# Optimization experiments

Hardware: AMD Instinct MI355X
Metric: run time of the kernel (lower is better)

Reference implementation:

```python
import jax, jax.numpy as jnp
import numpy as np

B, D, L, G, K, U, OUT = 131072, 256, 3, 4, 128, 64, 10


def setup_inputs() -> dict:
    key = jax.random.key(0)
    k1, k2, k3, k4 = jax.random.split(key, 4)
    x = jax.random.normal(k1, (B, D), dtype=jnp.float32)
    # per-level, per-group input node coords into the previous level's output
    idx = jax.random.randint(k2, (L, G, K), 0, D, dtype=jnp.int32)
    # per-group kernels [fan_in, units] and biases [units], stacked
    W = jax.random.normal(k3, (L, G, K, U), dtype=jnp.float32) * 0.1
    b = jnp.zeros((L, G, U), dtype=jnp.float32)
    W_out = jax.random.normal(k4, (D, OUT), dtype=jnp.float32) * 0.1
    b_out = jnp.zeros((OUT,), dtype=jnp.float32)
    return {"x": x, "idx": idx, "W": W, "b": b, "W_out": W_out, "b_out": b_out}


def reference(x, idx, W, b, W_out, b_out):
    # Each topological level: for every dependency-group g, gather K scalar
    # columns from the previous level (the per-node slice+concat in the
    # original), tiny matmul [B,K]@[K,U] + bias, tanh; level output is the
    # concat of group outputs -> [B, G*U]. Groups share shapes, so they are
    # batched over axis g with a single einsum per level.
    h = x
    n_levels = W.shape[0]
    for l in range(n_levels):  # small fixed loop over topology levels
        gathered = h[:, idx[l]]                                  # [B, G, K]
        z = jnp.einsum('bgk,gku->bgu', gathered, W[l]) + b[l]    # [B, G, U]
        h = jnp.tanh(z).reshape(z.shape[0], -1)                  # [B, G*U]
    # output level: single group fed by all previous nodes, linear out activation
    return h @ W_out + b_out                                      # [B, OUT]
```

## Files before the change

### kernel.cpp

```cpp
#include <hip/hip_runtime.h>

typedef unsigned short ushort_t;
typedef __attribute__((ext_vector_type(8))) short short8;
typedef __attribute__((ext_vector_type(4))) float floatx4;

#define DD 256
#define LL 3
#define GG 4
#define KK 128
#define UU 64
#define OUTN 10
#define HSTRIDE 264
#define MROWS 64

__device__ __forceinline__ ushort_t f2bf(float f) {
  unsigned u = __builtin_bit_cast(unsigned, f);
  u = (u + 0x7FFFu + ((u >> 16) & 1u)) >> 16;
  return (ushort_t)u;
}

__device__ __forceinline__ unsigned pack_bf2(float lo, float hi) {
  unsigned a = __builtin_bit_cast(unsigned, hi) + 0x8000u;
  unsigned b = __builtin_bit_cast(unsigned, lo) + 0x8000u;
  return __builtin_amdgcn_perm(a, b, 0x07060302u);
}

__device__ __forceinline__ float fast_tanh(float x) {
  float e = __builtin_amdgcn_exp2f(x * 2.885390081777927f);
  return __builtin_fmaf(-2.0f, __builtin_amdgcn_rcpf(e + 1.0f), 1.0f);
}

__global__ __launch_bounds__(256) void prep_kernel(
    const int* __restrict__ idx, const float* __restrict__ W,
    const float* __restrict__ Wout, ushort_t* __restrict__ AT,
    ushort_t* __restrict__ WoT) {
  int b = blockIdx.x;
  int t = threadIdx.x;
  if (b < LL * DD) {
    int l = b >> 8, n = b & 255, g = n >> 6, u = n & 63;
    __shared__ int sidx[KK];
    __shared__ float sw[KK];
    if (t < KK) {
      sidx[t] = idx[(l * GG + g) * KK + t];
      sw[t]   = W[((size_t)((l * GG + g) * KK + t)) * UU + u];
    }
    __syncthreads();
    float s = 0.f;
#pragma unroll 8
    for (int j = 0; j < KK; j++) s += (sidx[j] == t) ? sw[j] : 0.f;
    AT[(b << 8) | t] = f2bf(s);
  } else {
    int e2 = (b - LL * DD) * 256 + t;
    int n = e2 >> 8, k = e2 & 255;
    WoT[e2] = (n < OUTN) ? f2bf(Wout[k * OUTN + n]) : (ushort_t)0;
  }
}

__global__ __launch_bounds__(256, 4) void fused_kernel(
    const float* __restrict__ x, const float* __restrict__ bias,
    const float* __restrict__ bout, const ushort_t* __restrict__ AT,
    const ushort_t* __restrict__ WoT, float* __restrict__ out) {
  __shared__ ushort_t hbuf[MROWS * HSTRIDE];

  const int tid  = threadIdx.x;
  const int wave = tid >> 6;
  const int lane = tid & 63;
  const int quad = lane >> 4;
  const int l16  = lane & 15;
  const long row0 = (long)blockIdx.x * MROWS;

  const float4* xv = (const float4*)(x + row0 * DD);
#pragma unroll
  for (int i = 0; i < 16; i++) {
    int f  = tid + i * 256;
    int r  = f >> 6;
    int c4 = f & 63;
    float4 v = xv[r * 64 + c4];
    uint2 w;
    w.x = pack_bf2(v.x, v.y);
    w.y = pack_bf2(v.z, v.w);
    *(uint2*)&hbuf[r * HSTRIDE + c4 * 4] = w;
  }
  __syncthreads();

#pragma unroll 1
  for (int l = 0; l < 3; l++) {
    const ushort_t* Ab = AT + l * (DD * DD) + (wave * UU + l16) * DD + quad * 8;
    const ushort_t* hsrc = hbuf + l16 * HSTRIDE + quad * 8;

    floatx4 acc[4][4];
#pragma unroll
    for (int nt = 0; nt < 4; nt++) {
      float4 bv = *(const float4*)&bias[(l * GG + wave) * UU + nt * 16 + quad * 4];
      floatx4 ini = {bv.x, bv.y, bv.z, bv.w};
#pragma unroll
      for (int mt = 0; mt < 4; mt++) acc[mt][nt] = ini;
    }

    short8 wf[4], wfn[4];
#pragma unroll
    for (int nt = 0; nt < 4; nt++) wf[nt] = *(const short8*)&Ab[nt * 16 * DD];

#pragma unroll
    for (int ks = 0; ks < 8; ks++) {
      if (ks < 7) {
#pragma unroll
        for (int nt = 0; nt < 4; nt++)
          wfn[nt] = *(const short8*)&Ab[nt * 16 * DD + (ks + 1) * 32];
      }
      short8 bfc = *(const short8*)&hsrc[0 * 16 * HSTRIDE + ks * 32];
#pragma unroll
      for (int mt = 0; mt < 4; mt++) {
        short8 bfn;
        if (mt < 3) bfn = *(const short8*)&hsrc[(mt + 1) * 16 * HSTRIDE + ks * 32];
#pragma unroll
        for (int nt = 0; nt < 4; nt++)
          acc[mt][nt] = __builtin_amdgcn_mfma_f32_16x16x32_bf16(wf[nt], bfc, acc[mt][nt], 0, 0, 0);
        bfc = bfn;
      }
#pragma unroll
      for (int nt = 0; nt < 4; nt++) wf[nt] = wfn[nt];
    }
    __syncthreads();

#pragma unroll
    for (int nt = 0; nt < 4; nt++) {
#pragma unroll
      for (int mt = 0; mt < 4; mt++) {
        uint2 w;
        w.x = pack_bf2(fast_tanh(acc[mt][nt][0]), fast_tanh(acc[mt][nt][1]));
        w.y = pack_bf2(fast_tanh(acc[mt][nt][2]), fast_tanh(acc[mt][nt][3]));
        *(uint2*)&hbuf[(mt * 16 + l16) * HSTRIDE + wave * UU + nt * 16 + quad * 4] = w;
      }
    }
    __syncthreads();
  }

  short8 wof[8];
#pragma unroll
  for (int ks = 0; ks < 8; ks++)
    wof[ks] = *(const short8*)&WoT[l16 * DD + ks * 32 + quad * 8];

  floatx4 accf = {0.f, 0.f, 0.f, 0.f};
#pragma unroll
  for (int ks = 0; ks < 8; ks++) {
    short8 bfr = *(const short8*)&hbuf[(wave * 16 + l16) * HSTRIDE + ks * 32 + quad * 8];
    accf = __builtin_amdgcn_mfma_f32_16x16x32_bf16(wof[ks], bfr, accf, 0, 0, 0);
  }
  const long obase = (row0 + wave * 16 + l16) * OUTN;
  if (quad < 2) {
    float4 p = {accf[0] + bout[quad * 4 + 0], accf[1] + bout[quad * 4 + 1],
                accf[2] + bout[quad * 4 + 2], accf[3] + bout[quad * 4 + 3]};
    *(float4*)&out[obase + quad * 4] = p;
  } else if (quad == 2) {
    float2 p = {accf[0] + bout[8], accf[1] + bout[9]};
    *(float2*)&out[obase + 8] = p;
  }
}

extern "C" void kernel_launch(void* const* d_in, const int* in_sizes, int n_in,
                              void* d_out, int out_size, void* d_ws, size_t ws_size,
                              hipStream_t stream) {
  const float* x    = (const float*)d_in[0];
  const int*   idx  = (const int*)d_in[1];
  const float* W    = (const float*)d_in[2];
  const float* b    = (const float*)d_in[3];
  const float* Wout = (const float*)d_in[4];
  const float* bout = (const float*)d_in[5];
  float* out = (float*)d_out;

  ushort_t* AT  = (ushort_t*)d_ws;
  ushort_t* WoT = AT + LL * DD * DD;

  prep_kernel<<<LL * DD + 16, 256, 0, stream>>>(idx, W, Wout, AT, WoT);
  fused_kernel<<<131072 / MROWS, 256, 0, stream>>>(x, b, bout, AT, WoT, out);
}
```

Baseline: 302.9 us.

## Split fused MLP into per-level kernels with bf16 global intermediates

```diff
diff --git a/kernel.cpp b/kernel.cpp
--- a/kernel.cpp
+++ b/kernel.cpp
@@ -11,7 +11,7 @@
 #define UU 64
 #define OUTN 10
 #define HSTRIDE 264
-#define MROWS 64
+#define BB 131072
 
 __device__ __forceinline__ ushort_t f2bf(float f) {
   unsigned u = __builtin_bit_cast(unsigned, f);
@@ -56,23 +56,188 @@
   }
 }
 
-__global__ __launch_bounds__(256, 4) void fused_kernel(
-    const float* __restrict__ x, const float* __restrict__ bias,
-    const float* __restrict__ bout, const ushort_t* __restrict__ AT,
-    const ushort_t* __restrict__ WoT, float* __restrict__ out) {
-  __shared__ ushort_t hbuf[MROWS * HSTRIDE];
-
+
+__global__ __launch_bounds__(512, 3) void level_f32(
+    const float* __restrict__ xin, const float* __restrict__ bias,
+    const ushort_t* __restrict__ A, ushort_t* __restrict__ hout) {
+  const int tid  = threadIdx.x;
+  const int wave = tid >> 6;
+  const int wm   = wave >> 2;
+  const int wn   = wave & 3;
+  const int lane = tid & 63;
+  const int quad = lane >> 4;
+  const int l16  = lane & 15;
+  const long row0 = (long)blockIdx.x * 128 + wm * 64;
+
+  const float*    xrow = xin + (row0 + l16) * DD + quad * 8;
+  const ushort_t* Ab   = A + (wn * 64 + l16) * DD + quad * 8;
+
+  floatx4 acc[4][4];
+#pragma unroll
+  for (int nt = 0; nt < 4; nt++) {
+    float4 bv = *(const float4*)&bias[wn * 64 + nt * 16 + quad * 4];
+    floatx4 ini = {bv.x, bv.y, bv.z, bv.w};
+#pragma unroll
+    for (int mt = 0; mt < 4; mt++) acc[mt][nt] = ini;
+  }
+
+  short8 wf[4], wfn[4];
+#pragma unroll
+  for (int nt = 0; nt < 4; nt++) wf[nt] = *(const short8*)&Ab[nt * 16 * DD];
+
+#pragma unroll
+  for (int ks = 0; ks < 8; ks++) {
+    if (ks < 7) {
+#pragma unroll
+      for (int nt = 0; nt < 4; nt++)
+        wfn[nt] = *(const short8*)&Ab[nt * 16 * DD + (ks + 1) * 32];
+    }
+    short8 af[4];
+#pragma unroll
+    for (int mt = 0; mt < 4; mt++) {
+      float4 v0 = *(const float4*)&xrow[mt * 16 * DD + ks * 32];
+      float4 v1 = *(const float4*)&xrow[mt * 16 * DD + ks * 32 + 4];
+      uint4 p;
+      p.x = pack_bf2(v0.x, v0.y); p.y = pack_bf2(v0.z, v0.w);
+      p.z = pack_bf2(v1.x, v1.y); p.w = pack_bf2(v1.z, v1.w);
+      af[mt] = __builtin_bit_cast(short8, p);
+    }
+#pragma unroll
+    for (int mt = 0; mt < 4; mt++)
+#pragma unroll
+      for (int nt = 0; nt < 4; nt++)
+        acc[mt][nt] = __builtin_amdgcn_mfma_f32_16x16x32_bf16(wf[nt], af[mt], acc[mt][nt], 0, 0, 0);
+#pragma unroll
+    for (int nt = 0; nt < 4; nt++) wf[nt] = wfn[nt];
+  }
+
+#pragma unroll
+  for (int mt = 0; mt < 4; mt++) {
+    ushort_t* hrow = hout + (row0 + mt * 16 + l16) * DD + wn * 64 + quad * 4;
+#pragma unroll
+    for (int nt = 0; nt < 4; nt++) {
+      uint2 w;
+      w.x = pack_bf2(fast_tanh(acc[mt][nt][0]), fast_tanh(acc[mt][nt][1]));
+      w.y = pack_bf2(fast_tanh(acc[mt][nt][2]), fast_tanh(acc[mt][nt][3]));
+      *(uint2*)&hrow[nt * 16] = w;
+    }
+  }
+}
+
+__global__ __launch_bounds__(512, 3) void level_bf16(
+    const ushort_t* __restrict__ hin, const float* __restrict__ bias,
+    const ushort_t* __restrict__ A, ushort_t* __restrict__ hout) {
+  const int tid  = threadIdx.x;
+  const int wave = tid >> 6;
+  const int wm   = wave >> 2;
+  const int wn   = wave & 3;
+  const int lane = tid & 63;
+  const int quad = lane >> 4;
+  const int l16  = lane & 15;
+  const long row0 = (long)blockIdx.x * 128 + wm * 64;
+
+  const ushort_t* hrow = hin + (row0 + l16) * DD + quad * 8;
+  const ushort_t* Ab   = A + (wn * 64 + l16) * DD + quad * 8;
+
+  floatx4 acc[4][4];
+#pragma unroll
+  for (int nt = 0; nt < 4; nt++) {
+    float4 bv = *(const float4*)&bias[wn * 64 + nt * 16 + quad * 4];
+    floatx4 ini = {bv.x, bv.y, bv.z, bv.w};
+#pragma unroll
+    for (int mt = 0; mt < 4; mt++) acc[mt][nt] = ini;
+  }
+
+  short8 wf[4], wfn[4], af[4], afn[4];
+#pragma unroll
+  for (int nt = 0; nt < 4; nt++) wf[nt] = *(const short8*)&Ab[nt * 16 * DD];
+#pragma unroll
+  for (int mt = 0; mt < 4; mt++) af[mt] = *(const short8*)&hrow[mt * 16 * DD];
+
+#pragma unroll
+  for (int ks = 0; ks < 8; ks++) {
+    if (ks < 7) {
+#pragma unroll
+      for (int nt = 0; nt < 4; nt++)
+        wfn[nt] = *(const short8*)&Ab[nt * 16 * DD + (ks + 1) * 32];
+#pragma unroll
+      for (int mt = 0; mt < 4; mt++)
+        afn[mt] = *(const short8*)&hrow[mt * 16 * DD + (ks + 1) * 32];
+    }
+#pragma unroll
+    for (int mt = 0; mt < 4; mt++)
+#pragma unroll
+      for (int nt = 0; nt < 4; nt++)
+        acc[mt][nt] = __builtin_amdgcn_mfma_f32_16x16x32_bf16(wf[nt], af[mt], acc[mt][nt], 0, 0, 0);
+#pragma unroll
+    for (int nt = 0; nt < 4; nt++) wf[nt] = wfn[nt];
+#pragma unroll
+    for (int mt = 0; mt < 4; mt++) af[mt] = afn[mt];
+  }
+
+#pragma unroll
+  for (int mt = 0; mt < 4; mt++) {
+    ushort_t* orow = hout + (row0 + mt * 16 + l16) * DD + wn * 64 + quad * 4;
+#pragma unroll
+    for (int nt = 0; nt < 4; nt++) {
+      uint2 w;
+      w.x = pack_bf2(fast_tanh(acc[mt][nt][0]), fast_tanh(acc[mt][nt][1]));
+      w.y = pack_bf2(fast_tanh(acc[mt][nt][2]), fast_tanh(acc[mt][nt][3]));
+      *(uint2*)&orow[nt * 16] = w;
+    }
+  }
+}
+
+__global__ __launch_bounds__(512, 4) void final_kernel(
+    const ushort_t* __restrict__ h3, const ushort_t* __restrict__ WoT,
+    const float* __restrict__ bout, float* __restrict__ out) {
   const int tid  = threadIdx.x;
   const int wave = tid >> 6;
   const int lane = tid & 63;
   const int quad = lane >> 4;
   const int l16  = lane & 15;
-  const long row0 = (long)blockIdx.x * MROWS;
+  const long row = (long)blockIdx.x * 128 + wave * 16 + l16;
+
+  const ushort_t* hrow = h3 + row * DD + quad * 8;
+
+  short8 wof[8];
+#pragma unroll
+  for (int ks = 0; ks < 8; ks++)
+    wof[ks] = *(const short8*)&WoT[l16 * DD + ks * 32 + quad * 8];
+
+  floatx4 accf = {0.f, 0.f, 0.f, 0.f};
+#pragma unroll
+  for (int ks = 0; ks < 8; ks++) {
+    short8 af = *(const short8*)&hrow[ks * 32];
+    accf = __builtin_amdgcn_mfma_f32_16x16x32_bf16(wof[ks], af, accf, 0, 0, 0);
+  }
+  const long obase = row * OUTN;
+  if (quad < 2) {
+    float4 p = {accf[0] + bout[quad * 4 + 0], accf[1] + bout[quad * 4 + 1],
+                accf[2] + bout[quad * 4 + 2], accf[3] + bout[quad * 4 + 3]};
+    *(float4*)&out[obase + quad * 4] = p;
+  } else if (quad == 2) {
+    float2 p = {accf[0] + bout[8], accf[1] + bout[9]};
+    *(float2*)&out[obase + 8] = p;
+  }
+}
+
+__global__ __launch_bounds__(512, 4) void fused_fallback(
+    const float* __restrict__ x, const float* __restrict__ bias,
+    const float* __restrict__ bout, const ushort_t* __restrict__ AT,
+    const ushort_t* __restrict__ WoT, float* __restrict__ out) {
+  __shared__ ushort_t hbuf[128 * HSTRIDE];
+  const int tid  = threadIdx.x;
+  const int wave = tid >> 6;
+  const int lane = tid & 63;
+  const int quad = lane >> 4;
+  const int l16  = lane & 15;
+  const long row0 = (long)blockIdx.x * 128;
 
   const float4* xv = (const float4*)(x + row0 * DD);
 #pragma unroll
   for (int i = 0; i < 16; i++) {
-    int f  = tid + i * 256;
+    int f  = tid + i * 512;
     int r  = f >> 6;
     int c4 = f & 63;
     float4 v = xv[r * 64 + c4];
@@ -85,52 +250,47 @@
 
 #pragma unroll 1
   for (int l = 0; l < 3; l++) {
-    const ushort_t* Ab = AT + l * (DD * DD) + (wave * UU + l16) * DD + quad * 8;
+    const ushort_t* Ab = AT + l * (DD * DD) + (wave * 32 + l16) * DD + quad * 8;
     const ushort_t* hsrc = hbuf + l16 * HSTRIDE + quad * 8;
-
-    floatx4 acc[4][4];
-#pragma unroll
-    for (int nt = 0; nt < 4; nt++) {
-      float4 bv = *(const float4*)&bias[(l * GG + wave) * UU + nt * 16 + quad * 4];
+    floatx4 acc[8][2];
+#pragma unroll
+    for (int nt = 0; nt < 2; nt++) {
+      float4 bv = *(const float4*)&bias[l * DD + wave * 32 + nt * 16 + quad * 4];
       floatx4 ini = {bv.x, bv.y, bv.z, bv.w};
 #pragma unroll
-      for (int mt = 0; mt < 4; mt++) acc[mt][nt] = ini;
-    }
-
-    short8 wf[4], wfn[4];
-#pragma unroll
-    for (int nt = 0; nt < 4; nt++) wf[nt] = *(const short8*)&Ab[nt * 16 * DD];
-
+      for (int mt = 0; mt < 8; mt++) acc[mt][nt] = ini;
+    }
+    short8 wf[2], wfn[2];
+#pragma unroll
+    for (int nt = 0; nt < 2; nt++) wf[nt] = *(const short8*)&Ab[nt * 16 * DD];
 #pragma unroll
     for (int ks = 0; ks < 8; ks++) {
       if (ks < 7) {
 #pragma unroll
-        for (int nt = 0; nt < 4; nt++)
+        for (int nt = 0; nt < 2; nt++)
           wfn[nt] = *(const short8*)&Ab[nt * 16 * DD + (ks + 1) * 32];
       }
-      short8 bfc = *(const short8*)&hsrc[0 * 16 * HSTRIDE + ks * 32];
-#pragma unroll
-      for (int mt = 0; mt < 4; mt++) {
+      short8 bfc = *(const short8*)&hsrc[ks * 32];
+#pragma unroll
+      for (int mt = 0; mt < 8; mt++) {
         short8 bfn;
-        if (mt < 3) bfn = *(const short8*)&hsrc[(mt + 1) * 16 * HSTRIDE + ks * 32];
-#pragma unroll
-        for (int nt = 0; nt < 4; nt++)
-          acc[mt][nt] = __builtin_amdgcn_mfma_f32_16x16x32_bf16(wf[nt], bfc, acc[mt][nt], 0, 0, 0);
+        if (mt < 7) bfn = *(const short8*)&hsrc[(mt + 1) * 16 * HSTRIDE + ks * 32];
+        acc[mt][0] = __builtin_amdgcn_mfma_f32_16x16x32_bf16(wf[0], bfc, acc[mt][0], 0, 0, 0);
+        acc[mt][1] = __builtin_amdgcn_mfma_f32_16x16x32_bf16(wf[1], bfc, acc[mt][1], 0, 0, 0);
         bfc = bfn;
       }
 #pragma unroll
-      for (int nt = 0; nt < 4; nt++) wf[nt] = wfn[nt];
+      for (int nt = 0; nt < 2; nt++) wf[nt] = wfn[nt];
     }
     __syncthreads();
-
-#pragma unroll
-    for (int nt = 0; nt < 4; nt++) {
-#pragma unroll
-      for (int mt = 0; mt < 4; mt++) {
+#pragma unroll
+    for (int nt = 0; nt < 2; nt++) {
+#pragma unroll
+      for (int mt = 0; mt < 8; mt++) {
         uint2 w;
         w.x = pack_bf2(fast_tanh(acc[mt][nt][0]), fast_tanh(acc[mt][nt][1]));
         w.y = pack_bf2(fast_tanh(acc[mt][nt][2]), fast_tanh(acc[mt][nt][3]));
-        *(uint2*)&hbuf[(mt * 16 + l16) * HSTRIDE + wave * UU + nt * 16 + quad * 4] = w;
+        *(uint2*)&hbuf[(mt * 16 + l16) * HSTRIDE + wave * 32 + nt * 16 + quad * 4] = w;
       }
     }
     __syncthreads();
@@ -140,7 +300,6 @@
 #pragma unroll
   for (int ks = 0; ks < 8; ks++)
     wof[ks] = *(const short8*)&WoT[l16 * DD + ks * 32 + quad * 8];
-
   floatx4 accf = {0.f, 0.f, 0.f, 0.f};
 #pragma unroll
   for (int ks = 0; ks < 8; ks++) {
@@ -172,6 +331,20 @@
   ushort_t* AT  = (ushort_t*)d_ws;
   ushort_t* WoT = AT + LL * DD * DD;
 
+  const size_t hbytes = (size_t)BB * DD * 2;
+  const size_t base   = 393216 + 8192;
+  const size_t needed = base + 2 * hbytes;
+
   prep_kernel<<<LL * DD + 16, 256, 0, stream>>>(idx, W, Wout, AT, WoT);
-  fused_kernel<<<131072 / MROWS, 256, 0, stream>>>(x, b, bout, AT, WoT, out);
-}
+
+  if (ws_size >= needed) {
+    ushort_t* hA = (ushort_t*)((char*)d_ws + base);
+    ushort_t* hB = (ushort_t*)((char*)d_ws + base + hbytes);
+    level_f32 <<<BB / 128, 512, 0, stream>>>(x,  b + 0 * DD, AT,                hA);
+    level_bf16<<<BB / 128, 512, 0, stream>>>(hA, b + 1 * DD, AT + 1 * DD * DD,  hB);
+    level_bf16<<<BB / 128, 512, 0, stream>>>(hB, b + 2 * DD, AT + 2 * DD * DD,  hA);
+    final_kernel<<<BB / 128, 512, 0, stream>>>(hA, WoT, bout, out);
+  } else {
+    fused_fallback<<<BB / 128, 512, 0, stream>>>(x, b, bout, AT, WoT, out);
+  }
+}
```

Measured after the change: 442.3 us. 1.46x slower.
